# Performance work log

Measured on AMD Instinct MI355X. Metric: run time of the kernel, lower is better.

The kernel has to match this reference:

```python
import jax, jax.numpy as jnp
import numpy as np


def setup_inputs() -> dict:
    key = jax.random.key(0)
    k1, k2, k3, k4 = jax.random.split(key, 4)
    B, C, T, H, W = 2, 64, 8, 48, 48
    C2 = C // 2
    x_in = jax.random.normal(k1, (B, C, T, H, W), dtype=jnp.float32)
    # per-time-slice 1x1 conv weights (theta/phi pairs), kaiming-ish scale
    theta_w = jax.random.normal(k2, (T, C2, C), dtype=jnp.float32) / np.sqrt(C)
    phi_w = jax.random.normal(k3, (T, C2, C), dtype=jnp.float32) / np.sqrt(C)
    out_w = jax.random.normal(k4, (C, C), dtype=jnp.float32) / np.sqrt(C)
    return {"x_in": x_in, "theta_w": theta_w, "phi_w": phi_w, "out_w": out_w}


def reference(x_in, theta_w, phi_w, out_w):
    B, C, T, H, W = x_in.shape
    C2 = theta_w.shape[1]
    P = H * W
    # [B, T, C, P] layout: flatten spatial, move time next to batch
    x = jnp.transpose(x_in, (0, 2, 1, 3, 4)).reshape(B, T, C, P)
    # per-slice 1x1 convs == per-slice channel matmuls with slice-specific weights
    theta = jnp.einsum("toc,btcp->btop", theta_w, x)  # [B,T,C2,P]
    phi = jnp.einsum("toc,btcp->btop", phi_w, x)      # [B,T,C2,P]
    scale = 1.0 / jnp.sqrt(jnp.asarray(C2, dtype=x_in.dtype))
    scores = jnp.einsum("btcp,btcq->btpq", theta, phi) * scale  # [B,T,P,P]
    attn = jax.nn.softmax(scores, axis=-1)
    f = jnp.einsum("btpq,btcq->btcp", attn, x)  # value = raw x, [B,T,C,P]
    # conv_out: 1x1x1 Conv3d (pointwise over channels), then residual
    out = jnp.einsum("oc,btcp->btop", out_w, f)
    out = jnp.transpose(out.reshape(B, T, C, H, W), (0, 2, 1, 3, 4))
    return out + x_in
```

## Files before the change

### kernel.cpp

```cpp
#include <hip/hip_runtime.h>
#include <hip/hip_bf16.h>

#define CC 64
#define TT 8
#define PP 2304
#define C2 32
#define BT 16
#define NKT 36
#define QKT 9
#define SCALE2 0.25503486f

using h8 = __attribute__((ext_vector_type(8))) _Float16;
using h4 = __attribute__((ext_vector_type(4))) _Float16;
using f4 = __attribute__((ext_vector_type(4))) float;

#if __has_builtin(__builtin_amdgcn_exp2f)
#define EXP2(v) __builtin_amdgcn_exp2f(v)
#else
#define EXP2(v) exp2f(v)
#endif

#define SWIZ_BT(xcd, g) ((xcd) + 8 * ((g) & 1))
#define SWIZ_PT(g) ((g) >> 1)


__global__ __launch_bounds__(256) void k_prep(
    const float* __restrict__ x, const float* __restrict__ tw,
    const float* __restrict__ pw, _Float16* __restrict__ thf,
    _Float16* __restrict__ rec) {
  const int qt = SWIZ_PT(blockIdx.y), bt = SWIZ_BT(blockIdx.x, blockIdx.y);
  const int b = bt >> 3, t = bt & 7;
  const int tid = threadIdx.x;
  const int wv = tid >> 6, lane = tid & 63;
  const int quad = lane >> 4, l15 = lane & 15;

  __shared__ __align__(16) float x_s[64][68];
  __shared__ __align__(16) _Float16 th_s[4][16][32];
  __shared__ __align__(16) _Float16 ph_s[4][16][32];

  const size_t xslice = ((size_t)b * CC * TT + t) * PP;
  const int qg0 = qt * 64;

  {
    const int l16 = tid & 15;
    const int crow = tid >> 4;
#pragma unroll
    for (int ppass = 0; ppass < 4; ppass++) {
      const int c = ppass * 16 + crow;
      float4 u = *reinterpret_cast<const float4*>(
          &x[xslice + (size_t)c * (TT * PP) + qg0 + l16 * 4]);
      x_s[l16 * 4 + 0][c] = u.x;
      x_s[l16 * 4 + 1][c] = u.y;
      x_s[l16 * 4 + 2][c] = u.z;
      x_s[l16 * 4 + 3][c] = u.w;
    }
  }
  __syncthreads();

  h8 bx[2];
#pragma unroll
  for (int ks = 0; ks < 2; ks++) {
    const float* row = &x_s[wv * 16 + l15][ks * 32 + quad * 8];
    float4 u0 = *reinterpret_cast<const float4*>(row);
    float4 u1 = *reinterpret_cast<const float4*>(row + 4);
    bx[ks][0] = (_Float16)u0.x; bx[ks][1] = (_Float16)u0.y;
    bx[ks][2] = (_Float16)u0.z; bx[ks][3] = (_Float16)u0.w;
    bx[ks][4] = (_Float16)u1.x; bx[ks][5] = (_Float16)u1.y;
    bx[ks][6] = (_Float16)u1.z; bx[ks][7] = (_Float16)u1.w;
  }

  const float* twt = tw + t * C2 * CC;
  const float* pwt = pw + t * C2 * CC;
  const f4 zero = {0.f, 0.f, 0.f, 0.f};
  f4 accT[2] = {zero, zero}, accP[2] = {zero, zero};
#pragma unroll
  for (int mt = 0; mt < 2; mt++)
#pragma unroll
    for (int ks = 0; ks < 2; ks++) {
      const float* wr = twt + (mt * 16 + l15) * CC + ks * 32 + quad * 8;
      const float* pr = pwt + (mt * 16 + l15) * CC + ks * 32 + quad * 8;
      float4 a0 = *reinterpret_cast<const float4*>(wr);
      float4 a1 = *reinterpret_cast<const float4*>(wr + 4);
      float4 p0 = *reinterpret_cast<const float4*>(pr);
      float4 p1 = *reinterpret_cast<const float4*>(pr + 4);
      h8 at = {(_Float16)a0.x, (_Float16)a0.y, (_Float16)a0.z, (_Float16)a0.w,
               (_Float16)a1.x, (_Float16)a1.y, (_Float16)a1.z, (_Float16)a1.w};
      h8 ap = {(_Float16)p0.x, (_Float16)p0.y, (_Float16)p0.z, (_Float16)p0.w,
               (_Float16)p1.x, (_Float16)p1.y, (_Float16)p1.z, (_Float16)p1.w};
      accT[mt] =
          __builtin_amdgcn_mfma_f32_16x16x32_f16(at, bx[ks], accT[mt], 0, 0, 0);
      accP[mt] =
          __builtin_amdgcn_mfma_f32_16x16x32_f16(ap, bx[ks], accP[mt], 0, 0, 0);
    }

#pragma unroll
  for (int mt = 0; mt < 2; mt++) {
    h4 tv, pv;
#pragma unroll
    for (int r = 0; r < 4; r++) {
      tv[r] = (_Float16)(accT[mt][r] * SCALE2);
      pv[r] = (_Float16)accP[mt][r];
    }
    *reinterpret_cast<h4*>(&th_s[wv][l15][mt * 16 + quad * 4]) = tv;
    *reinterpret_cast<h4*>(&ph_s[wv][l15][mt * 16 + quad * 4]) = pv;
  }

  h8 tfrag = *reinterpret_cast<const h8*>(&th_s[wv][l15][quad * 8]);
  *reinterpret_cast<h8*>(
      thf + (((size_t)(bt * NKT + qt) * 4 + wv) * 64 + lane) * 8) = tfrag;

  _Float16* rb = rec + (size_t)(bt * NKT + qt) * 6144;
  h8 pfrag = *reinterpret_cast<const h8*>(&ph_s[wv][l15][quad * 8]);
  *reinterpret_cast<h8*>(rb + wv * 512 + lane * 8) = pfrag;

  {
    const int g = wv >> 1;
#pragma unroll
    for (int ct2 = 0; ct2 < 2; ct2++) {
      const int ct = (wv & 1) * 2 + ct2;
      h8 v;
#pragma unroll
      for (int j = 0; j < 4; j++) {
        v[j] = (_Float16)x_s[32 * g + quad * 4 + j][ct * 16 + l15];
        v[4 + j] = (_Float16)x_s[32 * g + 16 + quad * 4 + j][ct * 16 + l15];
      }
      *reinterpret_cast<h8*>(rb + 2048 + (g * 4 + ct) * 512 + lane * 8) = v;
    }
  }
}

__global__ __launch_bounds__(256, 2) void k_attn(
    const float* __restrict__ x, const _Float16* __restrict__ thf,
    const _Float16* __restrict__ rec, const float* __restrict__ ow,
    float* __restrict__ out) {
  const int strip = SWIZ_PT(blockIdx.y);
  const int bt = SWIZ_BT(blockIdx.x, blockIdx.y);
  const int b = bt >> 3, t = bt & 7;
  const int tid = threadIdx.x;
  const int kg = tid >> 6, lane = tid & 63;
  const int quad = lane >> 4, l15 = lane & 15;

  __shared__ __align__(16) float exch[4 * 4 * 16 * 64];
  __shared__ float exl[4 * 4 * 64];

  h8 bth[4];
#pragma unroll
  for (int pf = 0; pf < 4; pf++)
    bth[pf] = *reinterpret_cast<const h8*>(
        thf + (((size_t)bt * 144 + strip * 4 + pf) * 64 + lane) * 8);

  const _Float16* recb =
      rec + ((size_t)bt * NKT + (size_t)kg * QKT) * 6144 + lane * 8;

  const f4 zero = {0.f, 0.f, 0.f, 0.f};
  f4 O[4][4];
#pragma unroll
  for (int ct = 0; ct < 4; ct++)
#pragma unroll
    for (int pf = 0; pf < 4; pf++) O[ct][pf] = zero;
  float lsum[4] = {0.f, 0.f, 0.f, 0.f};

  h8 Abuf[12], Bbuf[12];

#define LOADREC(BUF, kt)                                          \
  {                                                               \
    const _Float16* _p = recb + (size_t)(kt)*6144;                \
    _Pragma("unroll") for (int j = 0; j < 12; j++)                \
        BUF[j] = *reinterpret_cast<const h8*>(_p + j * 512);      \
  }

#define COMPUTE(BUF)                                                          \
  {                                                                           \
    _Pragma("unroll") for (int pf = 0; pf < 4; pf++) {                        \
      f4 s[4];                                                                \
      _Pragma("unroll") for (int nt = 0; nt < 4; nt++)                        \
          s[nt] = __builtin_amdgcn_mfma_f32_16x16x32_f16(BUF[nt], bth[pf],    \
                                                         zero, 0, 0, 0);     \
      _Pragma("unroll") for (int g = 0; g < 2; g++) {                         \
        h8 bw;                                                                \
        _Pragma("unroll") for (int r = 0; r < 4; r++) {                       \
          float w0 = EXP2(s[2 * g][r]);                                       \
          float w1 = EXP2(s[2 * g + 1][r]);                                   \
          lsum[pf] += w0 + w1;                                                \
          bw[r] = (_Float16)w0;                                               \
          bw[4 + r] = (_Float16)w1;                                           \
        }                                                                     \
        _Pragma("unroll") for (int ct = 0; ct < 4; ct++)                      \
            O[ct][pf] = __builtin_amdgcn_mfma_f32_16x16x32_f16(               \
                BUF[4 + g * 4 + ct], bw, O[ct][pf], 0, 0, 0);                 \
      }                                                                       \
    }                                                                         \
  }

  LOADREC(Abuf, 0);
#pragma unroll 1
  for (int i = 0; i < QKT - 1; i += 2) {
    LOADREC(Bbuf, i + 1);
    COMPUTE(Abuf);
    LOADREC(Abuf, i + 2);
    COMPUTE(Bbuf);
  }
  COMPUTE(Abuf);
#undef LOADREC
#undef COMPUTE

#pragma unroll
  for (int pf = 0; pf < 4; pf++) {
    lsum[pf] += __shfl_xor(lsum[pf], 16);
    lsum[pf] += __shfl_xor(lsum[pf], 32);
  }

#pragma unroll
  for (int pf = 0; pf < 4; pf++) {
#pragma unroll
    for (int ct = 0; ct < 4; ct++)
#pragma unroll
      for (int r = 0; r < 4; r++)
        exch[((kg * 4 + pf) * 16 + ct * 4 + r) * 64 + lane] = O[ct][pf][r];
    exl[(kg * 4 + pf) * 64 + lane] = lsum[pf];
  }
  __syncthreads();

  float ls = 0.f;
#pragma unroll
  for (int src = 0; src < 4; src++) ls += exl[(src * 4 + kg) * 64 + lane];
  const float inv = 1.f / ls;

  h4 bf[4];
#pragma unroll
  for (int ct = 0; ct < 4; ct++)
#pragma unroll
    for (int r = 0; r < 4; r++) {
      float acc = 0.f;
#pragma unroll
      for (int src = 0; src < 4; src++)
        acc += exch[((src * 4 + kg) * 16 + ct * 4 + r) * 64 + lane];
      bf[ct][r] = (_Float16)(acc * inv);
    }

  f4 D3[4] = {zero, zero, zero, zero};
#pragma unroll
  for (int mt = 0; mt < 4; mt++)
#pragma unroll
    for (int ct = 0; ct < 4; ct++) {
      const float* wrow = ow + (size_t)(mt * 16 + l15) * CC + ct * 16 + quad * 4;
      float4 u = *reinterpret_cast<const float4*>(wrow);
      h4 aw = {(_Float16)u.x, (_Float16)u.y, (_Float16)u.z, (_Float16)u.w};
      D3[mt] = __builtin_amdgcn_mfma_f32_16x16x16f16(aw, bf[ct], D3[mt], 0, 0, 0);
    }

  const int p0 = strip * 64 + kg * 16 + l15;
#pragma unroll
  for (int mt = 0; mt < 4; mt++)
#pragma unroll
    for (int r = 0; r < 4; r++) {
      const int o = mt * 16 + quad * 4 + r;
      const size_t base = ((size_t)(b * CC + o) * TT + t) * PP + p0;
      out[base] = D3[mt][r] + x[base];
    }
}

extern "C" void kernel_launch(void* const* d_in, const int* in_sizes, int n_in,
                              void* d_out, int out_size, void* d_ws,
                              size_t ws_size, hipStream_t stream) {
  (void)in_sizes; (void)n_in; (void)out_size; (void)ws_size;
  const float* x = (const float*)d_in[0];
  const float* tw = (const float*)d_in[1];
  const float* pw = (const float*)d_in[2];
  const float* ow = (const float*)d_in[3];
  float* out = (float*)d_out;

  _Float16* thf = (_Float16*)d_ws;
  _Float16* rec = thf + (size_t)BT * NKT * 4 * 64 * 8;

  k_prep<<<dim3(8, 72), 256, 0, stream>>>(x, tw, pw, thf, rec);
  k_attn<<<dim3(8, 72), 256, 0, stream>>>(x, thf, rec, ow, out);
}
```

Before: 104.7 us.

## Shrink attention query strip to 48 rows and raise occupancy to three blocks

Each attention block now handles 48 query positions (three fragments) instead of 64, and the grid grows from 72 to 96 strips per slice. The smaller register footprint allows launch bounds of three blocks per SM. The explicit A/B double-buffered key loads are replaced by a single fully unrolled buffer loop, leaving load overlap to the compiler. The cost is that each key tile is re-read by more blocks, and one of four waves sits idle during the output projection.

```diff
diff --git a/kernel.cpp b/kernel.cpp
--- a/kernel.cpp
+++ b/kernel.cpp
@@ -21,14 +21,13 @@
 #endif
 
 #define SWIZ_BT(xcd, g) ((xcd) + 8 * ((g) & 1))
-#define SWIZ_PT(g) ((g) >> 1)
 
 
 __global__ __launch_bounds__(256) void k_prep(
     const float* __restrict__ x, const float* __restrict__ tw,
     const float* __restrict__ pw, _Float16* __restrict__ thf,
     _Float16* __restrict__ rec) {
-  const int qt = SWIZ_PT(blockIdx.y), bt = SWIZ_BT(blockIdx.x, blockIdx.y);
+  const int qt = blockIdx.y >> 1, bt = SWIZ_BT(blockIdx.x, blockIdx.y);
   const int b = bt >> 3, t = bt & 7;
   const int tid = threadIdx.x;
   const int wv = tid >> 6, lane = tid & 63;
@@ -129,135 +128,130 @@
   }
 }
 
-__global__ __launch_bounds__(256, 2) void k_attn(
+__global__ __launch_bounds__(256, 3) void k_attn(
     const float* __restrict__ x, const _Float16* __restrict__ thf,
     const _Float16* __restrict__ rec, const float* __restrict__ ow,
     float* __restrict__ out) {
-  const int strip = SWIZ_PT(blockIdx.y);
+  const int strip = blockIdx.y >> 1;
   const int bt = SWIZ_BT(blockIdx.x, blockIdx.y);
   const int b = bt >> 3, t = bt & 7;
   const int tid = threadIdx.x;
   const int kg = tid >> 6, lane = tid & 63;
   const int quad = lane >> 4, l15 = lane & 15;
 
-  __shared__ __align__(16) float exch[4 * 4 * 16 * 64];
-  __shared__ float exl[4 * 4 * 64];
-
-  h8 bth[4];
-#pragma unroll
-  for (int pf = 0; pf < 4; pf++)
+  __shared__ __align__(16) float exch[4 * 3 * 16 * 64];
+  __shared__ float exl[4 * 3 * 64];
+
+  h8 bth[3];
+#pragma unroll
+  for (int pf = 0; pf < 3; pf++)
     bth[pf] = *reinterpret_cast<const h8*>(
-        thf + (((size_t)bt * 144 + strip * 4 + pf) * 64 + lane) * 8);
+        thf + (((size_t)bt * 144 + strip * 3 + pf) * 64 + lane) * 8);
 
   const _Float16* recb =
       rec + ((size_t)bt * NKT + (size_t)kg * QKT) * 6144 + lane * 8;
 
   const f4 zero = {0.f, 0.f, 0.f, 0.f};
-  f4 O[4][4];
+  f4 O[4][3];
 #pragma unroll
   for (int ct = 0; ct < 4; ct++)
 #pragma unroll
-    for (int pf = 0; pf < 4; pf++) O[ct][pf] = zero;
-  float lsum[4] = {0.f, 0.f, 0.f, 0.f};
-
-  h8 Abuf[12], Bbuf[12];
-
-#define LOADREC(BUF, kt)                                          \
-  {                                                               \
-    const _Float16* _p = recb + (size_t)(kt)*6144;                \
-    _Pragma("unroll") for (int j = 0; j < 12; j++)                \
-        BUF[j] = *reinterpret_cast<const h8*>(_p + j * 512);      \
-  }
-
-#define COMPUTE(BUF)                                                          \
-  {                                                                           \
-    _Pragma("unroll") for (int pf = 0; pf < 4; pf++) {                        \
-      f4 s[4];                                                                \
-      _Pragma("unroll") for (int nt = 0; nt < 4; nt++)                        \
-          s[nt] = __builtin_amdgcn_mfma_f32_16x16x32_f16(BUF[nt], bth[pf],    \
-                                                         zero, 0, 0, 0);     \
-      _Pragma("unroll") for (int g = 0; g < 2; g++) {                         \
-        h8 bw;                                                                \
-        _Pragma("unroll") for (int r = 0; r < 4; r++) {                       \
-          float w0 = EXP2(s[2 * g][r]);                                       \
-          float w1 = EXP2(s[2 * g + 1][r]);                                   \
-          lsum[pf] += w0 + w1;                                                \
-          bw[r] = (_Float16)w0;                                               \
-          bw[4 + r] = (_Float16)w1;                                           \
-        }                                                                     \
-        _Pragma("unroll") for (int ct = 0; ct < 4; ct++)                      \
-            O[ct][pf] = __builtin_amdgcn_mfma_f32_16x16x32_f16(               \
-                BUF[4 + g * 4 + ct], bw, O[ct][pf], 0, 0, 0);                 \
-      }                                                                       \
-    }                                                                         \
-  }
-
-  LOADREC(Abuf, 0);
-#pragma unroll 1
-  for (int i = 0; i < QKT - 1; i += 2) {
-    LOADREC(Bbuf, i + 1);
-    COMPUTE(Abuf);
-    LOADREC(Abuf, i + 2);
-    COMPUTE(Bbuf);
-  }
-  COMPUTE(Abuf);
-#undef LOADREC
-#undef COMPUTE
-
-#pragma unroll
-  for (int pf = 0; pf < 4; pf++) {
+    for (int pf = 0; pf < 3; pf++) O[ct][pf] = zero;
+  float lsum[3] = {0.f, 0.f, 0.f};
+
+  h8 buf[12];
+
+#pragma unroll
+  for (int i = 0; i < QKT; i++) {
+    const _Float16* _p = recb + (size_t)i * 6144;
+#pragma unroll
+    for (int j = 0; j < 12; j++)
+      buf[j] = *reinterpret_cast<const h8*>(_p + j * 512);
+
+#pragma unroll
+    for (int pf = 0; pf < 3; pf++) {
+      f4 s[4];
+#pragma unroll
+      for (int nt = 0; nt < 4; nt++)
+        s[nt] = __builtin_amdgcn_mfma_f32_16x16x32_f16(buf[nt], bth[pf], zero,
+                                                       0, 0, 0);
+#pragma unroll
+      for (int g = 0; g < 2; g++) {
+        h8 bw;
+#pragma unroll
+        for (int r = 0; r < 4; r++) {
+          float w0 = EXP2(s[2 * g][r]);
+          float w1 = EXP2(s[2 * g + 1][r]);
+          lsum[pf] += w0 + w1;
+          bw[r] = (_Float16)w0;
+          bw[4 + r] = (_Float16)w1;
+        }
+#pragma unroll
+        for (int ct = 0; ct < 4; ct++)
+          O[ct][pf] = __builtin_amdgcn_mfma_f32_16x16x32_f16(
+              buf[4 + g * 4 + ct], bw, O[ct][pf], 0, 0, 0);
+      }
+    }
+  }
+
+#pragma unroll
+  for (int pf = 0; pf < 3; pf++) {
     lsum[pf] += __shfl_xor(lsum[pf], 16);
     lsum[pf] += __shfl_xor(lsum[pf], 32);
   }
 
 #pragma unroll
-  for (int pf = 0; pf < 4; pf++) {
+  for (int pf = 0; pf < 3; pf++) {
 #pragma unroll
     for (int ct = 0; ct < 4; ct++)
 #pragma unroll
       for (int r = 0; r < 4; r++)
-        exch[((kg * 4 + pf) * 16 + ct * 4 + r) * 64 + lane] = O[ct][pf][r];
-    exl[(kg * 4 + pf) * 64 + lane] = lsum[pf];
+        exch[((kg * 3 + pf) * 16 + ct * 4 + r) * 64 + lane] = O[ct][pf][r];
+    exl[(kg * 3 + pf) * 64 + lane] = lsum[pf];
   }
   __syncthreads();
 
-  float ls = 0.f;
-#pragma unroll
-  for (int src = 0; src < 4; src++) ls += exl[(src * 4 + kg) * 64 + lane];
-  const float inv = 1.f / ls;
-
-  h4 bf[4];
-#pragma unroll
-  for (int ct = 0; ct < 4; ct++)
-#pragma unroll
-    for (int r = 0; r < 4; r++) {
-      float acc = 0.f;
-#pragma unroll
-      for (int src = 0; src < 4; src++)
-        acc += exch[((src * 4 + kg) * 16 + ct * 4 + r) * 64 + lane];
-      bf[ct][r] = (_Float16)(acc * inv);
-    }
-
-  f4 D3[4] = {zero, zero, zero, zero};
-#pragma unroll
-  for (int mt = 0; mt < 4; mt++)
-#pragma unroll
-    for (int ct = 0; ct < 4; ct++) {
-      const float* wrow = ow + (size_t)(mt * 16 + l15) * CC + ct * 16 + quad * 4;
-      float4 u = *reinterpret_cast<const float4*>(wrow);
-      h4 aw = {(_Float16)u.x, (_Float16)u.y, (_Float16)u.z, (_Float16)u.w};
-      D3[mt] = __builtin_amdgcn_mfma_f32_16x16x16f16(aw, bf[ct], D3[mt], 0, 0, 0);
-    }
-
-  const int p0 = strip * 64 + kg * 16 + l15;
-#pragma unroll
-  for (int mt = 0; mt < 4; mt++)
-#pragma unroll
-    for (int r = 0; r < 4; r++) {
-      const int o = mt * 16 + quad * 4 + r;
-      const size_t base = ((size_t)(b * CC + o) * TT + t) * PP + p0;
-      out[base] = D3[mt][r] + x[base];
-    }
+  if (kg < 3) {
+    float ls = 0.f;
+#pragma unroll
+    for (int src = 0; src < 4; src++) ls += exl[(src * 3 + kg) * 64 + lane];
+    const float inv = 1.f / ls;
+
+    h4 bf[4];
+#pragma unroll
+    for (int ct = 0; ct < 4; ct++)
+#pragma unroll
+      for (int r = 0; r < 4; r++) {
+        float acc = 0.f;
+#pragma unroll
+        for (int src = 0; src < 4; src++)
+          acc += exch[((src * 3 + kg) * 16 + ct * 4 + r) * 64 + lane];
+        bf[ct][r] = (_Float16)(acc * inv);
+      }
+
+    f4 D3[4] = {zero, zero, zero, zero};
+#pragma unroll
+    for (int mt = 0; mt < 4; mt++)
+#pragma unroll
+      for (int ct = 0; ct < 4; ct++) {
+        const float* wrow =
+            ow + (size_t)(mt * 16 + l15) * CC + ct * 16 + quad * 4;
+        float4 u = *reinterpret_cast<const float4*>(wrow);
+        h4 aw = {(_Float16)u.x, (_Float16)u.y, (_Float16)u.z, (_Float16)u.w};
+        D3[mt] =
+            __builtin_amdgcn_mfma_f32_16x16x16f16(aw, bf[ct], D3[mt], 0, 0, 0);
+      }
+
+    const int p0 = strip * 48 + kg * 16 + l15;
+#pragma unroll
+    for (int mt = 0; mt < 4; mt++)
+#pragma unroll
+      for (int r = 0; r < 4; r++) {
+        const int o = mt * 16 + quad * 4 + r;
+        const size_t base = ((size_t)(b * CC + o) * TT + t) * PP + p0;
+        out[base] = D3[mt][r] + x[base];
+      }
+  }
 }
 
 extern "C" void kernel_launch(void* const* d_in, const int* in_sizes, int n_in,
@@ -274,5 +268,5 @@
   _Float16* rec = thf + (size_t)BT * NKT * 4 * 64 * 8;
 
   k_prep<<<dim3(8, 72), 256, 0, stream>>>(x, tw, pw, thf, rec);
-  k_attn<<<dim3(8, 72), 256, 0, stream>>>(x, thf, rec, ow, out);
+  k_attn<<<dim3(8, 96), 256, 0, stream>>>(x, thf, rec, ow, out);
 }
```

Result: faster. 98.55 us (-5.8%).
